# Performance work log

Hardware: AMD Instinct MI355X
Metric: run time of the kernel (lower is better)

The kernel has to match this reference:

```python
import jax, jax.numpy as jnp
import numpy as np

B, S, D, H = 4, 2048, 1024, 16
DH = D // H


def setup_inputs() -> dict:
    key = jax.random.key(0)
    k1, k2, k3, k4, k5 = jax.random.split(key, 5)
    x = jax.random.normal(k1, (B, S, D), dtype=jnp.float32)
    mask = jnp.tril(jnp.ones((S, S), dtype=bool))  # causal mask
    scale = 1.0 / np.sqrt(D)
    w_qkv = jax.random.normal(k2, (D, 3 * D), dtype=jnp.float32) * scale
    b_qkv = jnp.zeros((3 * D,), dtype=jnp.float32)
    w_out = jax.random.normal(k3, (D, D), dtype=jnp.float32) * scale
    b_out = jnp.zeros((D,), dtype=jnp.float32)
    return {"x": x, "w_qkv": w_qkv, "b_qkv": b_qkv, "w_out": w_out, "b_out": b_out, "mask": mask}


def reference(x, w_qkv, b_qkv, w_out, b_out, mask):
    qkv = jnp.einsum('bsd,de->bse', x, w_qkv) + b_qkv  # (B,S,3D)
    q, k, v = jnp.split(qkv, 3, axis=-1)
    # (B,S,D) -> (B,H,S,DH)
    q = q.reshape(B, S, H, DH).transpose(0, 2, 1, 3)
    k = k.reshape(B, S, H, DH).transpose(0, 2, 1, 3)
    v = v.reshape(B, S, H, DH).transpose(0, 2, 1, 3)
    scores = jnp.einsum('bhqd,bhkd->bhqk', q, k) / jnp.sqrt(jnp.float32(DH))
    scores = jnp.where(mask[None, None, :, :], scores, -jnp.inf)
    attn = jax.nn.softmax(scores, axis=-1)  # dropout p=0.0 -> identity
    out = jnp.einsum('bhqk,bhkd->bhqd', attn, v)
    out = out.transpose(0, 2, 1, 3).reshape(B, S, D)
    return jnp.einsum('bsd,de->bse', out, w_out) + b_out
```

## Files before the change

kernel.cpp:

```cpp
#include <hip/hip_runtime.h>
#include <hip/hip_bf16.h>

typedef unsigned short u16;
typedef __bf16 bf16x8 __attribute__((ext_vector_type(8)));
typedef float f32x4 __attribute__((ext_vector_type(4)));
typedef unsigned short u16x8 __attribute__((ext_vector_type(8)));

__device__ __forceinline__ void async_copy16(void* lds, const void* g) {
  __builtin_amdgcn_global_load_lds(
      (const __attribute__((address_space(1))) unsigned int*)g,
      (__attribute__((address_space(3))) unsigned int*)lds, 16, 0, 0);
}

__device__ __forceinline__ u16 f2bf(float f) {
  __hip_bfloat16 h = __float2bfloat16(f);
  u16 u;
  __builtin_memcpy(&u, &h, 2);
  return u;
}

__device__ __forceinline__ u16 f2bf_rne(float f) {
  unsigned b = __builtin_bit_cast(unsigned, f);
  b += 0x7FFF + ((b >> 16) & 1);
  return (u16)(b >> 16);
}

__device__ __forceinline__ unsigned cvt_pk_bf16(float a, float b) {
  unsigned r;
  asm("v_cvt_pk_bf16_f32 %0, %1, %2" : "=v"(r) : "v"(a), "v"(b));
  return r;
}

__global__ void k_f32_to_bf16(const float* __restrict__ in, u16* __restrict__ out, int n4) {
  int i = blockIdx.x * blockDim.x + threadIdx.x;
  if (i >= n4) return;
  float4 v = ((const float4*)in)[i];
  ushort4 o;
  o.x = f2bf(v.x); o.y = f2bf(v.y); o.z = f2bf(v.z); o.w = f2bf(v.w);
  ((ushort4*)out)[i] = o;
}

__global__ void k_transpose_bf16(const float* __restrict__ in, u16* __restrict__ out, int R, int C) {
  __shared__ float tile[32][33];
  int bx = blockIdx.x * 32;
  int by = blockIdx.y * 32;
  int tx = threadIdx.x & 31, ty = threadIdx.x >> 5;
  for (int i = ty; i < 32; i += 8) tile[i][tx] = in[(size_t)(by + i) * C + bx + tx];
  __syncthreads();
  for (int i = ty; i < 32; i += 8) out[(size_t)(bx + i) * R + by + tx] = f2bf(tile[tx][i]);
}

template <int OUT_BF16>
__global__ __launch_bounds__(256, 2) void k_gemm_bt(
    const u16* __restrict__ A, const u16* __restrict__ Bt,
    const float* __restrict__ bias, void* __restrict__ Cout,
    int M, int N, int K) {
  __shared__ __align__(16) u16 As[128][32];
  __shared__ __align__(16) u16 Bs[128][32];
  const int t = threadIdx.x;
  const int l = t & 63, w = t >> 6;
  const int lr = l & 15, lk = l >> 4;
  const int wr = w >> 1, wc = w & 1;
  const int m0 = blockIdx.x * 128, n0 = blockIdx.y * 128;

  f32x4 acc[4][4] = {};

  for (int k0 = 0; k0 < K; k0 += 32) {
    __syncthreads();
    for (int c = 0; c < 2; ++c) {
      int idx = c * 256 + t;
      int row = idx >> 2, slot = idx & 3;
      int sw = (slot ^ ((row >> 1) & 3)) << 3;
      async_copy16((char*)&As[0][0] + idx * 16, A + (size_t)(m0 + row) * K + k0 + sw);
      async_copy16((char*)&Bs[0][0] + idx * 16, Bt + (size_t)(n0 + row) * K + k0 + sw);
    }
    __syncthreads();
    bf16x8 af[4], bfr[4];
    for (int m = 0; m < 4; ++m) {
      int row = wr * 64 + m * 16 + lr;
      af[m] = *(const bf16x8*)((const char*)&As[0][0] + row * 64 + ((lk ^ ((row >> 1) & 3)) << 4));
    }
    for (int n = 0; n < 4; ++n) {
      int row = wc * 64 + n * 16 + lr;
      bfr[n] = *(const bf16x8*)((const char*)&Bs[0][0] + row * 64 + ((lk ^ ((row >> 1) & 3)) << 4));
    }
    for (int m = 0; m < 4; ++m)
      for (int n = 0; n < 4; ++n)
        acc[m][n] = __builtin_amdgcn_mfma_f32_16x16x32_bf16(af[m], bfr[n], acc[m][n], 0, 0, 0);
  }

  for (int n = 0; n < 4; ++n) {
    int col = n0 + wc * 64 + n * 16 + lr;
    float bv = bias[col];
    for (int m = 0; m < 4; ++m) {
      int rowb = m0 + wr * 64 + m * 16 + lk * 4;
      for (int r = 0; r < 4; ++r) {
        float v = acc[m][n][r] + bv;
        size_t off = (size_t)(rowb + r) * N + col;
        if constexpr (OUT_BF16) ((u16*)Cout)[off] = f2bf(v);
        else ((float*)Cout)[off] = v;
      }
    }
  }
}

__global__ __launch_bounds__(256, 4) void k_attn(
    const u16* __restrict__ QKV,
    u16* __restrict__ O) {
  const int bh = blockIdx.x;
  const int p = blockIdx.y;
  const int b = bh >> 4, h = bh & 15;
  const int t = threadIdx.x;
  const int l = t & 63, w = t >> 6;
  const int lr = l & 15, lk = l >> 4;
  constexpr float LG = 0.18033688f;

  __shared__ __align__(16) u16 Ks[2][64][64];
  __shared__ __align__(16) u16 VT[2][64][64];
  __shared__ __align__(16) u16 Pl[4][16][64];

  const u16* Kb0 = QKV + (size_t)b * 2048 * 3072 + 1024 + h * 64;
  const u16* Vb0 = Kb0 + 1024;

  u16x8 vreg[2];

  auto stageK = [&](int j, int buf) {
#pragma unroll
    for (int c = 0; c < 2; ++c) {
      int gi = c * 256 + t;
      int row = gi >> 3, slot = gi & 7;
      async_copy16((char*)&Ks[buf][0][0] + gi * 16,
                   Kb0 + ((size_t)j * 64 + row) * 3072 + ((slot ^ (row & 7)) << 3));
    }
  };
  auto loadV = [&](int j) {
#pragma unroll
    for (int c = 0; c < 2; ++c) {
      int r = c * 32 + (t >> 3), dh0 = (t & 7) << 3;
      vreg[c] = *(const u16x8*)(Vb0 + ((size_t)j * 64 + r) * 3072 + dh0);
    }
  };
  auto writeV = [&](int buf) {
#pragma unroll
    for (int c = 0; c < 2; ++c) {
      int r = c * 32 + (t >> 3), dh0 = (t & 7) << 3;
#pragma unroll
      for (int jj = 0; jj < 8; ++jj) {
        int dh = dh0 + jj;
        int phi = (dh & 7) ^ ((dh >> 3) & 7);
        VT[buf][dh][((((r >> 3) ^ phi) & 7) << 3) | (r & 7)] = vreg[c][jj];
      }
    }
  };

  auto run_tile = [&](int qt) {
    const int nt = qt + 1;
    const int q0w = qt * 64 + w * 16;
    const size_t rowQ = (size_t)b * 2048 + q0w;

    bf16x8 qf[2];
#pragma unroll
    for (int c = 0; c < 2; ++c)
      qf[c] = *(const bf16x8*)(QKV + (rowQ + lr) * 3072 + h * 64 + c * 32 + lk * 8);

    f32x4 acc[4] = {};
    float mi = -__builtin_inff(), li = 0.f;

    stageK(0, 0);
    loadV(0);
    writeV(0);
    __syncthreads();

    for (int j = 0; j < nt; ++j) {
      const int cur = j & 1;
      const bool more = (j + 1 < nt);
      if (more) { stageK(j + 1, cur ^ 1); loadV(j + 1); }

      f32x4 s[4] = {};
#pragma unroll
      for (int c = 0; c < 2; ++c)
#pragma unroll
        for (int n = 0; n < 4; ++n) {
          int row = n * 16 + lr;
          bf16x8 kf = *(const bf16x8*)((const char*)&Ks[cur][0][0] + row * 128 +
                                       ((((c * 4 + lk) ^ (row & 7)) & 7) << 4));
          s[n] = __builtin_amdgcn_mfma_f32_16x16x32_bf16(kf, qf[c], s[n], 0, 0, 0);
        }

      if (j * 64 + 63 > q0w) {
        const int kb = j * 64 + lk * 4;
        const int qq = q0w + lr;
#pragma unroll
        for (int n = 0; n < 4; ++n)
#pragma unroll
          for (int r = 0; r < 4; ++r)
            if (kb + n * 16 + r > qq) s[n][r] = -__builtin_inff();
      }

      float tm;
      {
        float m0 = fmaxf(fmaxf(s[0][0], s[0][1]), fmaxf(s[0][2], s[0][3]));
        float m1 = fmaxf(fmaxf(s[1][0], s[1][1]), fmaxf(s[1][2], s[1][3]));
        float m2 = fmaxf(fmaxf(s[2][0], s[2][1]), fmaxf(s[2][2], s[2][3]));
        float m3 = fmaxf(fmaxf(s[3][0], s[3][1]), fmaxf(s[3][2], s[3][3]));
        tm = fmaxf(fmaxf(m0, m1), fmaxf(m2, m3));
        tm = fmaxf(tm, __shfl_xor(tm, 16));
        tm = fmaxf(tm, __shfl_xor(tm, 32));
      }
      if (__any(tm > mi + 64.0f)) {
        float mnew = fmaxf(mi, tm);
        float alpha = __builtin_amdgcn_exp2f((mi - mnew) * LG);
        mi = mnew;
        li *= alpha;
        float a0 = __shfl(alpha, lk * 4 + 0);
        float a1 = __shfl(alpha, lk * 4 + 1);
        float a2 = __shfl(alpha, lk * 4 + 2);
        float a3 = __shfl(alpha, lk * 4 + 3);
#pragma unroll
        for (int n = 0; n < 4; ++n) {
          acc[n][0] *= a0; acc[n][1] *= a1; acc[n][2] *= a2; acc[n][3] *= a3;
        }
      }

      u16* pw = &Pl[w][0][0];
      {
        const float mc = -mi * LG;
        float ps = 0.f;
#pragma unroll
        for (int n = 0; n < 4; ++n) {
          float p0 = __builtin_amdgcn_exp2f(fmaf(s[n][0], LG, mc));
          float p1 = __builtin_amdgcn_exp2f(fmaf(s[n][1], LG, mc));
          float p2 = __builtin_amdgcn_exp2f(fmaf(s[n][2], LG, mc));
          float p3 = __builtin_amdgcn_exp2f(fmaf(s[n][3], LG, mc));
          ps += (p0 + p1) + (p2 + p3);
          unsigned w0 = cvt_pk_bf16(p0, p1);
          unsigned w1 = cvt_pk_bf16(p2, p3);
          int kc = (n * 2 + (lk >> 1)) ^ (lr & 7);
          *(uint2*)(pw + lr * 64 + kc * 8 + (lk & 1) * 4) = make_uint2(w0, w1);
        }
        ps += __shfl_xor(ps, 16);
        ps += __shfl_xor(ps, 32);
        li += ps;
      }

#pragma unroll
      for (int c = 0; c < 2; ++c) {
        bf16x8 pa = *(const bf16x8*)(pw + lr * 64 + (((c * 4 + lk) ^ (lr & 7)) << 3));
#pragma unroll
        for (int n = 0; n < 4; ++n) {
          int dh = n * 16 + lr;
          int phi = (dh & 7) ^ ((dh >> 3) & 7);
          bf16x8 vf = *(const bf16x8*)((const char*)&VT[cur][0][0] + dh * 128 +
                                       ((((c * 4 + lk) ^ phi) & 7) << 4));
          acc[n] = __builtin_amdgcn_mfma_f32_16x16x32_bf16(pa, vf, acc[n], 0, 0, 0);
        }
      }

      if (more) writeV(cur ^ 1);
      __syncthreads();
    }

    float l0 = __shfl(li, lk * 4 + 0);
    float l1 = __shfl(li, lk * 4 + 1);
    float l2 = __shfl(li, lk * 4 + 2);
    float l3 = __shfl(li, lk * 4 + 3);
    float inv[4] = {1.0f / l0, 1.0f / l1, 1.0f / l2, 1.0f / l3};
#pragma unroll
    for (int r = 0; r < 4; ++r) {
      size_t orow = (rowQ + lk * 4 + r) * 1024 + h * 64;
#pragma unroll
      for (int n = 0; n < 4; ++n) O[orow + n * 16 + lr] = f2bf_rne(acc[n][r] * inv[r]);
    }
  };

  run_tile(31 - p);
  run_tile(p);
}

extern "C" void kernel_launch(void* const* d_in, const int* in_sizes, int n_in,
                              void* d_out, int out_size, void* d_ws, size_t ws_size,
                              hipStream_t stream) {
  const float* x = (const float*)d_in[0];
  const float* w_qkv = (const float*)d_in[1];
  const float* b_qkv = (const float*)d_in[2];
  const float* w_out = (const float*)d_in[3];
  const float* b_out = (const float*)d_in[4];

  char* ws = (char*)d_ws;
  u16* X16 = (u16*)(ws);
  u16* WqkvT = (u16*)(ws + 16777216);
  u16* WoutT = (u16*)(ws + 23068672);
  u16* QKVb = (u16*)(ws + 25165824);
  u16* O16 = X16;

  k_f32_to_bf16<<<8192, 256, 0, stream>>>(x, X16, 8388608 / 4);
  k_transpose_bf16<<<dim3(96, 32), 256, 0, stream>>>(w_qkv, WqkvT, 1024, 3072);
  k_transpose_bf16<<<dim3(32, 32), 256, 0, stream>>>(w_out, WoutT, 1024, 1024);
  k_gemm_bt<1><<<dim3(64, 24), 256, 0, stream>>>(X16, WqkvT, b_qkv, QKVb, 8192, 3072, 1024);
  k_attn<<<dim3(64, 16), 256, 0, stream>>>(QKVb, O16);
  k_gemm_bt<0><<<dim3(64, 8), 256, 0, stream>>>(O16, WoutT, b_out, d_out, 8192, 1024, 1024);
}
```

Measured before the change: 188.3 us.

## Double attention query tile per warp to reuse K/V fragments across two row groups

```diff
diff --git a/kernel.cpp b/kernel.cpp
--- a/kernel.cpp
+++ b/kernel.cpp
@@ -104,7 +104,7 @@
   }
 }
 
-__global__ __launch_bounds__(256, 4) void k_attn(
+__global__ __launch_bounds__(256, 3) void k_attn(
     const u16* __restrict__ QKV,
     u16* __restrict__ O) {
   const int bh = blockIdx.x;
@@ -117,7 +117,7 @@
 
   __shared__ __align__(16) u16 Ks[2][64][64];
   __shared__ __align__(16) u16 VT[2][64][64];
-  __shared__ __align__(16) u16 Pl[4][16][64];
+  __shared__ __align__(16) u16 Pl[4][32][64];
 
   const u16* Kb0 = QKV + (size_t)b * 2048 * 3072 + 1024 + h * 64;
   const u16* Vb0 = Kb0 + 1024;
@@ -154,17 +154,21 @@
   };
 
   auto run_tile = [&](int qt) {
-    const int nt = qt + 1;
-    const int q0w = qt * 64 + w * 16;
+    const int nt = 2 * qt + 2;
+    const int q0w = qt * 128 + w * 32;
     const size_t rowQ = (size_t)b * 2048 + q0w;
 
-    bf16x8 qf[2];
-#pragma unroll
-    for (int c = 0; c < 2; ++c)
-      qf[c] = *(const bf16x8*)(QKV + (rowQ + lr) * 3072 + h * 64 + c * 32 + lk * 8);
-
-    f32x4 acc[4] = {};
-    float mi = -__builtin_inff(), li = 0.f;
+    bf16x8 qf[2][2];
+#pragma unroll
+    for (int g = 0; g < 2; ++g)
+#pragma unroll
+      for (int c = 0; c < 2; ++c)
+        qf[g][c] = *(const bf16x8*)(QKV + (rowQ + g * 16 + lr) * 3072 + h * 64 + c * 32 + lk * 8);
+
+    f32x4 acc[2][4] = {};
+    float mi[2], li[2];
+#pragma unroll
+    for (int g = 0; g < 2; ++g) { mi[g] = -__builtin_inff(); li[g] = 0.f; }
 
     stageK(0, 0);
     loadV(0);
@@ -176,7 +180,7 @@
       const bool more = (j + 1 < nt);
       if (more) { stageK(j + 1, cur ^ 1); loadV(j + 1); }
 
-      f32x4 s[4] = {};
+      f32x4 s[2][4] = {};
 #pragma unroll
       for (int c = 0; c < 2; ++c)
 #pragma unroll
@@ -184,75 +188,87 @@
           int row = n * 16 + lr;
           bf16x8 kf = *(const bf16x8*)((const char*)&Ks[cur][0][0] + row * 128 +
                                        ((((c * 4 + lk) ^ (row & 7)) & 7) << 4));
-          s[n] = __builtin_amdgcn_mfma_f32_16x16x32_bf16(kf, qf[c], s[n], 0, 0, 0);
+          s[0][n] = __builtin_amdgcn_mfma_f32_16x16x32_bf16(kf, qf[0][c], s[0][n], 0, 0, 0);
+          s[1][n] = __builtin_amdgcn_mfma_f32_16x16x32_bf16(kf, qf[1][c], s[1][n], 0, 0, 0);
         }
 
       if (j * 64 + 63 > q0w) {
         const int kb = j * 64 + lk * 4;
-        const int qq = q0w + lr;
-#pragma unroll
-        for (int n = 0; n < 4; ++n)
-#pragma unroll
-          for (int r = 0; r < 4; ++r)
-            if (kb + n * 16 + r > qq) s[n][r] = -__builtin_inff();
-      }
-
-      float tm;
-      {
-        float m0 = fmaxf(fmaxf(s[0][0], s[0][1]), fmaxf(s[0][2], s[0][3]));
-        float m1 = fmaxf(fmaxf(s[1][0], s[1][1]), fmaxf(s[1][2], s[1][3]));
-        float m2 = fmaxf(fmaxf(s[2][0], s[2][1]), fmaxf(s[2][2], s[2][3]));
-        float m3 = fmaxf(fmaxf(s[3][0], s[3][1]), fmaxf(s[3][2], s[3][3]));
-        tm = fmaxf(fmaxf(m0, m1), fmaxf(m2, m3));
-        tm = fmaxf(tm, __shfl_xor(tm, 16));
-        tm = fmaxf(tm, __shfl_xor(tm, 32));
-      }
-      if (__any(tm > mi + 64.0f)) {
-        float mnew = fmaxf(mi, tm);
-        float alpha = __builtin_amdgcn_exp2f((mi - mnew) * LG);
-        mi = mnew;
-        li *= alpha;
-        float a0 = __shfl(alpha, lk * 4 + 0);
-        float a1 = __shfl(alpha, lk * 4 + 1);
-        float a2 = __shfl(alpha, lk * 4 + 2);
-        float a3 = __shfl(alpha, lk * 4 + 3);
+#pragma unroll
+        for (int g = 0; g < 2; ++g) {
+          const int qq = q0w + g * 16 + lr;
+#pragma unroll
+          for (int n = 0; n < 4; ++n)
+#pragma unroll
+            for (int r = 0; r < 4; ++r)
+              if (kb + n * 16 + r > qq) s[g][n][r] = -__builtin_inff();
+        }
+      }
+
+      float tm[2];
+#pragma unroll
+      for (int g = 0; g < 2; ++g) {
+        float m0 = fmaxf(fmaxf(s[g][0][0], s[g][0][1]), fmaxf(s[g][0][2], s[g][0][3]));
+        float m1 = fmaxf(fmaxf(s[g][1][0], s[g][1][1]), fmaxf(s[g][1][2], s[g][1][3]));
+        float m2 = fmaxf(fmaxf(s[g][2][0], s[g][2][1]), fmaxf(s[g][2][2], s[g][2][3]));
+        float m3 = fmaxf(fmaxf(s[g][3][0], s[g][3][1]), fmaxf(s[g][3][2], s[g][3][3]));
+        float x = fmaxf(fmaxf(m0, m1), fmaxf(m2, m3));
+        x = fmaxf(x, __shfl_xor(x, 16));
+        x = fmaxf(x, __shfl_xor(x, 32));
+        tm[g] = x;
+      }
+      if (__any((tm[0] > mi[0] + 64.0f) || (tm[1] > mi[1] + 64.0f))) {
+#pragma unroll
+        for (int g = 0; g < 2; ++g) {
+          float mnew = fmaxf(mi[g], tm[g]);
+          float alpha = __builtin_amdgcn_exp2f((mi[g] - mnew) * LG);
+          mi[g] = mnew;
+          li[g] *= alpha;
+          float a0 = __shfl(alpha, lk * 4 + 0);
+          float a1 = __shfl(alpha, lk * 4 + 1);
+          float a2 = __shfl(alpha, lk * 4 + 2);
+          float a3 = __shfl(alpha, lk * 4 + 3);
+#pragma unroll
+          for (int n = 0; n < 4; ++n) {
+            acc[g][n][0] *= a0; acc[g][n][1] *= a1; acc[g][n][2] *= a2; acc[g][n][3] *= a3;
+          }
+        }
+      }
+
+      u16* pw = &Pl[w][0][0];
+#pragma unroll
+      for (int g = 0; g < 2; ++g) {
+        const float mc = -mi[g] * LG;
+        float ps = 0.f;
 #pragma unroll
         for (int n = 0; n < 4; ++n) {
-          acc[n][0] *= a0; acc[n][1] *= a1; acc[n][2] *= a2; acc[n][3] *= a3;
-        }
-      }
-
-      u16* pw = &Pl[w][0][0];
-      {
-        const float mc = -mi * LG;
-        float ps = 0.f;
-#pragma unroll
-        for (int n = 0; n < 4; ++n) {
-          float p0 = __builtin_amdgcn_exp2f(fmaf(s[n][0], LG, mc));
-          float p1 = __builtin_amdgcn_exp2f(fmaf(s[n][1], LG, mc));
-          float p2 = __builtin_amdgcn_exp2f(fmaf(s[n][2], LG, mc));
-          float p3 = __builtin_amdgcn_exp2f(fmaf(s[n][3], LG, mc));
+          float p0 = __builtin_amdgcn_exp2f(fmaf(s[g][n][0], LG, mc));
+          float p1 = __builtin_amdgcn_exp2f(fmaf(s[g][n][1], LG, mc));
+          float p2 = __builtin_amdgcn_exp2f(fmaf(s[g][n][2], LG, mc));
+          float p3 = __builtin_amdgcn_exp2f(fmaf(s[g][n][3], LG, mc));
           ps += (p0 + p1) + (p2 + p3);
           unsigned w0 = cvt_pk_bf16(p0, p1);
           unsigned w1 = cvt_pk_bf16(p2, p3);
           int kc = (n * 2 + (lk >> 1)) ^ (lr & 7);
-          *(uint2*)(pw + lr * 64 + kc * 8 + (lk & 1) * 4) = make_uint2(w0, w1);
+          *(uint2*)(pw + (g * 16 + lr) * 64 + kc * 8 + (lk & 1) * 4) = make_uint2(w0, w1);
         }
         ps += __shfl_xor(ps, 16);
         ps += __shfl_xor(ps, 32);
-        li += ps;
+        li[g] += ps;
       }
 
 #pragma unroll
       for (int c = 0; c < 2; ++c) {
-        bf16x8 pa = *(const bf16x8*)(pw + lr * 64 + (((c * 4 + lk) ^ (lr & 7)) << 3));
+        bf16x8 pa0 = *(const bf16x8*)(pw + lr * 64 + (((c * 4 + lk) ^ (lr & 7)) << 3));
+        bf16x8 pa1 = *(const bf16x8*)(pw + (16 + lr) * 64 + (((c * 4 + lk) ^ (lr & 7)) << 3));
 #pragma unroll
         for (int n = 0; n < 4; ++n) {
           int dh = n * 16 + lr;
           int phi = (dh & 7) ^ ((dh >> 3) & 7);
           bf16x8 vf = *(const bf16x8*)((const char*)&VT[cur][0][0] + dh * 128 +
                                        ((((c * 4 + lk) ^ phi) & 7) << 4));
-          acc[n] = __builtin_amdgcn_mfma_f32_16x16x32_bf16(pa, vf, acc[n], 0, 0, 0);
+          acc[0][n] = __builtin_amdgcn_mfma_f32_16x16x32_bf16(pa0, vf, acc[0][n], 0, 0, 0);
+          acc[1][n] = __builtin_amdgcn_mfma_f32_16x16x32_bf16(pa1, vf, acc[1][n], 0, 0, 0);
         }
       }
 
@@ -260,20 +276,23 @@
       __syncthreads();
     }
 
-    float l0 = __shfl(li, lk * 4 + 0);
-    float l1 = __shfl(li, lk * 4 + 1);
-    float l2 = __shfl(li, lk * 4 + 2);
-    float l3 = __shfl(li, lk * 4 + 3);
-    float inv[4] = {1.0f / l0, 1.0f / l1, 1.0f / l2, 1.0f / l3};
-#pragma unroll
-    for (int r = 0; r < 4; ++r) {
-      size_t orow = (rowQ + lk * 4 + r) * 1024 + h * 64;
-#pragma unroll
-      for (int n = 0; n < 4; ++n) O[orow + n * 16 + lr] = f2bf_rne(acc[n][r] * inv[r]);
+#pragma unroll
+    for (int g = 0; g < 2; ++g) {
+      float l0 = __shfl(li[g], lk * 4 + 0);
+      float l1 = __shfl(li[g], lk * 4 + 1);
+      float l2 = __shfl(li[g], lk * 4 + 2);
+      float l3 = __shfl(li[g], lk * 4 + 3);
+      float inv[4] = {1.0f / l0, 1.0f / l1, 1.0f / l2, 1.0f / l3};
+#pragma unroll
+      for (int r = 0; r < 4; ++r) {
+        size_t orow = (rowQ + g * 16 + lk * 4 + r) * 1024 + h * 64;
+#pragma unroll
+        for (int n = 0; n < 4; ++n) O[orow + n * 16 + lr] = f2bf_rne(acc[g][n][r] * inv[r]);
+      }
     }
   };
 
-  run_tile(31 - p);
+  run_tile(15 - p);
   run_tile(p);
 }
 
@@ -297,6 +316,6 @@
   k_transpose_bf16<<<dim3(96, 32), 256, 0, stream>>>(w_qkv, WqkvT, 1024, 3072);
   k_transpose_bf16<<<dim3(32, 32), 256, 0, stream>>>(w_out, WoutT, 1024, 1024);
   k_gemm_bt<1><<<dim3(64, 24), 256, 0, stream>>>(X16, WqkvT, b_qkv, QKVb, 8192, 3072, 1024);
-  k_attn<<<dim3(64, 16), 256, 0, stream>>>(QKVb, O16);
+  k_attn<<<dim3(64, 8), 256, 0, stream>>>(QKVb, O16);
   k_gemm_bt<0><<<dim3(64, 8), 256, 0, stream>>>(O16, WoutT, b_out, d_out, 8192, 1024, 1024);
 }
```

Measured after the change: 185.7 us. About the same (-1.3%).
